# Performance work log

Measured on AMD Instinct MI355X. Metric: run time of the kernel, lower is better.

The kernel has to match this reference:

```python
import jax, jax.numpy as jnp
import numpy as np

B, L, H, N = 4, 4096, 1024, 16
EPS = 1e-6  # layer_norm_epsilon


def setup_inputs() -> dict:
    key = jax.random.key(0)
    ks = jax.random.split(key, 8)
    hidden_states = jax.random.normal(ks[0], (B, L, H), dtype=jnp.float32)
    attention_mask = jnp.ones((B, L), dtype=jnp.float32)
    norm_weight = jnp.ones((H,), dtype=jnp.float32)
    # S4D init: dt log-uniform in [1e-3, 1e-1]; S4D-Lin A init; random C, D
    dt_min, dt_max = 1e-3, 1e-1
    log_dt = jax.random.uniform(ks[1], (H,), dtype=jnp.float32) * (
        float(np.log(dt_max)) - float(np.log(dt_min))) + float(np.log(dt_min))
    log_A_real = jnp.log(0.5 * jnp.ones((H, N), dtype=jnp.float32))
    A_imag = jnp.broadcast_to(float(np.pi) * jnp.arange(N, dtype=jnp.float32), (H, N))
    C_real = jax.random.normal(ks[2], (H, N), dtype=jnp.float32) * (0.5 ** 0.5)
    C_imag = jax.random.normal(ks[3], (H, N), dtype=jnp.float32) * (0.5 ** 0.5)
    D = jax.random.normal(ks[4], (H,), dtype=jnp.float32)
    out_w = jax.random.normal(ks[5], (2 * H, H), dtype=jnp.float32) * 0.02  # 1x1 conv to 2H (GLU)
    out_b = jnp.zeros((2 * H,), dtype=jnp.float32)
    return dict(hidden_states=hidden_states, attention_mask=attention_mask,
                norm_weight=norm_weight, log_dt=log_dt, log_A_real=log_A_real,
                A_imag=A_imag, C_real=C_real, C_imag=C_imag, D=D,
                out_w=out_w, out_b=out_b)


def _s4d_kernel(log_dt, log_A_real, A_imag, C_real, C_imag, length):
    """Diagonal SSM convolution kernel k[h, l] (S4D ZOH discretization)."""
    dt = jnp.exp(log_dt)                                   # (H,)
    A = -jnp.exp(log_A_real) + 1j * A_imag                 # (H, N) complex64
    C = C_real + 1j * C_imag                               # (H, N)
    dtA = A * dt[:, None]                                  # (H, N)
    C_disc = C * (jnp.exp(dtA) - 1.0) / A                  # (H, N)
    vand = jnp.exp(dtA[:, :, None] * jnp.arange(length, dtype=jnp.float32))  # (H, N, L)
    k = 2.0 * jnp.einsum('hn,hnl->hl', C_disc, vand).real  # (H, L)
    return k.astype(jnp.float32)


def reference(hidden_states, attention_mask, norm_weight, log_dt, log_A_real,
              A_imag, C_real, C_imag, D, out_w, out_b):
    # LongT5LayerNorm: RMSNorm (no mean subtraction), variance in fp32
    var = jnp.mean(jnp.square(hidden_states.astype(jnp.float32)), axis=-1, keepdims=True)
    normed = hidden_states * jax.lax.rsqrt(var + EPS) * norm_weight  # (B, L, H)
    # mask padded positions, go to channel-major layout (B, H, L)
    u = (normed * attention_mask[..., None]).transpose(0, 2, 1)
    Lx = u.shape[-1]
    k = _s4d_kernel(log_dt, log_A_real, A_imag, C_real, C_imag, Lx)  # (H, L)
    # causal convolution via FFT of length 2L
    nfft = 2 * Lx
    k_f = jnp.fft.rfft(k, n=nfft)                 # (H, nfft//2+1)
    u_f = jnp.fft.rfft(u, n=nfft)                 # (B, H, nfft//2+1)
    y = jnp.fft.irfft(u_f * k_f, n=nfft)[..., :Lx]  # (B, H, L)
    y = y + u * D[:, None]                        # skip connection
    y = jax.nn.gelu(y, approximate=False)         # torch nn.GELU (exact)
    # output 1x1 conv to 2H, then GLU over the channel dim
    z = jnp.einsum('bhl,oh->bol', y, out_w) + out_b[:, None]
    a, b = jnp.split(z, 2, axis=1)
    ssm_out = (a * jax.nn.sigmoid(b)).transpose(0, 2, 1)  # (B, L, H)
    # residual + dropout (eval mode -> identity)
    return hidden_states + ssm_out
```

## Files before the change

kernel.cpp:

```cpp
#include <hip/hip_runtime.h>

#define B_   4
#define L_   4096
#define H_   1024
#define N_   16
#define CH_  128
#define NC_  (L_/CH_)
#define M_   (B_*L_)
#define O2_  (2*H_)
#define EPS_ 1e-6f

typedef __attribute__((ext_vector_type(4))) float  f32x4;
typedef __attribute__((ext_vector_type(8))) __bf16 bf16x8;

__device__ __forceinline__ unsigned short f2bf(float x) {
  union { float f; unsigned int u; } v; v.f = x;
  unsigned int r = v.u + 0x7FFFu + ((v.u >> 16) & 1u);
  return (unsigned short)(r >> 16);
}

__device__ __forceinline__ void async_copy16(const void* g, void* l) {
  __builtin_amdgcn_global_load_lds(
      (const __attribute__((address_space(1))) unsigned int*)g,
      (__attribute__((address_space(3))) unsigned int*)l, 16, 0, 0);
}

__global__ void k_prep(const float* __restrict__ log_dt,
                       const float* __restrict__ log_A_real,
                       const float* __restrict__ A_imag,
                       const float* __restrict__ C_real,
                       const float* __restrict__ C_imag,
                       const float* __restrict__ outw,
                       const float* __restrict__ outb,
                       float* __restrict__ wr,  float* __restrict__ wi,
                       float* __restrict__ c2r, float* __restrict__ c2i,
                       float* __restrict__ wpr, float* __restrict__ wpi,
                       unsigned short* __restrict__ Wbf,
                       float* __restrict__ bp) {
  int idx = blockIdx.x * 256 + threadIdx.x;
  int p = idx >> 10, hh = idx & (H_ - 1);
  size_t src = (size_t)((p >> 1) + (p & 1) * H_) * H_ + hh;
  Wbf[idx] = f2bf(outw[src]);
  if (idx < O2_) bp[idx] = outb[(idx >> 1) + (idx & 1) * H_];
  if (idx < H_ * N_) {
    int h = idx / N_, n = idx % N_;
    int hn = h * N_ + n;
    float dt  = expf(log_dt[h]);
    float Ar  = -expf(log_A_real[hn]);
    float Ai  = A_imag[hn];
    float dr  = Ar * dt, di = Ai * dt;
    float er  = expf(dr);
    float wrv = er * cosf(di), wiv = er * sinf(di);
    float e1r = wrv - 1.0f, e1i = wiv;
    float den = Ar * Ar + Ai * Ai;
    float qr  = (e1r * Ar + e1i * Ai) / den;
    float qi  = (e1i * Ar - e1r * Ai) / den;
    float Cr  = C_real[hn], Ci = C_imag[hn];
    float cdr = Cr * qr - Ci * qi;
    float cdi = Cr * qi + Ci * qr;
    float ep  = expf((float)CH_ * dr);
    int o = n * H_ + h;
    wr[o]  = wrv;  wi[o]  = wiv;
    c2r[o] = 2.0f * cdr; c2i[o] = 2.0f * cdi;
    wpr[o] = ep * cosf((float)CH_ * di);
    wpi[o] = ep * sinf((float)CH_ * di);
  }
}

__global__ __launch_bounds__(256) void k_scale(const float* __restrict__ hs,
                                               const float* __restrict__ mask,
                                               float* __restrict__ scale) {
  int m = blockIdx.x, tid = threadIdx.x;
  float4 v = reinterpret_cast<const float4*>(hs + (size_t)m * H_)[tid];
  float s = v.x * v.x + v.y * v.y + v.z * v.z + v.w * v.w;
  #pragma unroll
  for (int off = 32; off > 0; off >>= 1) s += __shfl_down(s, off, 64);
  __shared__ float ps[4];
  if ((tid & 63) == 0) ps[tid >> 6] = s;
  __syncthreads();
  if (tid == 0) {
    float var = (ps[0] + ps[1] + ps[2] + ps[3]) * (1.0f / H_);
    scale[m] = rsqrtf(var + EPS_) * mask[m];
  }
}

__global__ __launch_bounds__(256) void k_scan1(const float* __restrict__ hs,
                                               const float* __restrict__ nw,
                                               const float* __restrict__ scale,
                                               const float* __restrict__ wr_,
                                               const float* __restrict__ wi_,
                                               float* __restrict__ endr,
                                               float* __restrict__ endi) {
  int tid = threadIdx.x;
  int h = blockIdx.x * 256 + tid;
  int c = blockIdx.y, b = blockIdx.z;
  float wr[N_], wi[N_], xr[N_], xi[N_];
  #pragma unroll
  for (int n = 0; n < N_; n++) {
    wr[n] = wr_[n * H_ + h]; wi[n] = wi_[n * H_ + h];
    xr[n] = 0.f; xi[n] = 0.f;
  }
  float nwh = nw[h];
  __shared__ float ssc[CH_];
  int l0 = c * CH_;
  if (tid < CH_) ssc[tid] = scale[(size_t)b * L_ + l0 + tid];
  __syncthreads();
  const float* hp = hs + ((size_t)b * L_ + l0) * H_ + h;
  #pragma unroll 8
  for (int l = 0; l < CH_; l++) {
    float u = hp[(size_t)l * H_] * ssc[l] * nwh;
    #pragma unroll
    for (int n = 0; n < N_; n++) {
      float oxr = xr[n];
      xr[n] = fmaf(wr[n], oxr, fmaf(-wi[n], xi[n], u));
      xi[n] = fmaf(wr[n], xi[n], wi[n] * oxr);
    }
  }
  size_t base = (((size_t)b * NC_ + c) * N_) * H_ + h;
  #pragma unroll
  for (int n = 0; n < N_; n++) {
    endr[base + (size_t)n * H_] = xr[n];
    endi[base + (size_t)n * H_] = xi[n];
  }
}

__global__ __launch_bounds__(256) void k_carry(const float* __restrict__ wpr_,
                                               const float* __restrict__ wpi_,
                                               const float* __restrict__ endr,
                                               const float* __restrict__ endi,
                                               float* __restrict__ carr,
                                               float* __restrict__ cari) {
  int idx = blockIdx.x * 256 + threadIdx.x;
  int h = idx & (H_ - 1);
  int n = (idx >> 10) & (N_ - 1);
  int b = idx >> 14;
  float wprv = wpr_[n * H_ + h], wpiv = wpi_[n * H_ + h];
  float sr = 0.f, si = 0.f;
  size_t cstride = (size_t)N_ * H_;
  size_t base = ((size_t)b * NC_) * cstride + (size_t)n * H_ + h;
  for (int c = 0; c < NC_; c++, base += cstride) {
    carr[base] = sr; cari[base] = si;
    float er = endr[base], ei = endi[base];
    float osr = sr;
    sr = fmaf(wprv, osr,  fmaf(-wpiv, si, er));
    si = fmaf(wprv, si, fmaf(wpiv, osr, ei));
  }
}

__global__ __launch_bounds__(256) void k_scan2(const float* __restrict__ hs,
                                               const float* __restrict__ nw,
                                               const float* __restrict__ scale,
                                               const float* __restrict__ wr_,
                                               const float* __restrict__ wi_,
                                               const float* __restrict__ c2r_,
                                               const float* __restrict__ c2i_,
                                               const float* __restrict__ Dp,
                                               const float* __restrict__ carr,
                                               const float* __restrict__ cari,
                                               unsigned short* __restrict__ ybf) {
  int tid = threadIdx.x;
  int h = blockIdx.x * 256 + tid;
  int c = blockIdx.y, b = blockIdx.z;
  float wr[N_], wi[N_], cr[N_], ci[N_], xr[N_], xi[N_];
  size_t base = (((size_t)b * NC_ + c) * N_) * H_ + h;
  #pragma unroll
  for (int n = 0; n < N_; n++) {
    wr[n] = wr_[n * H_ + h]; wi[n] = wi_[n * H_ + h];
    cr[n] = c2r_[n * H_ + h]; ci[n] = c2i_[n * H_ + h];
    xr[n] = carr[base + (size_t)n * H_];
    xi[n] = cari[base + (size_t)n * H_];
  }
  float nwh = nw[h], Dh = Dp[h];
  __shared__ float ssc[CH_];
  int l0 = c * CH_;
  if (tid < CH_) ssc[tid] = scale[(size_t)b * L_ + l0 + tid];
  __syncthreads();
  const float* hp = hs + ((size_t)b * L_ + l0) * H_ + h;
  unsigned short* yp = ybf + ((size_t)b * L_ + l0) * H_ + h;
  #pragma unroll 4
  for (int l = 0; l < CH_; l++) {
    float u = hp[(size_t)l * H_] * ssc[l] * nwh;
    float yv = u * Dh;
    #pragma unroll
    for (int n = 0; n < N_; n++) {
      float oxr = xr[n];
      xr[n] = fmaf(wr[n], oxr, fmaf(-wi[n], xi[n], u));
      xi[n] = fmaf(wr[n], xi[n], wi[n] * oxr);
      yv = fmaf(cr[n], xr[n], yv);
      yv = fmaf(-ci[n], xi[n], yv);
    }
    float g = 0.5f * yv * (1.0f + erff(yv * 0.70710678118654752f));
    yp[(size_t)l * H_] = f2bf(g);
  }
}

#define BM 128
#define BN 128
#define BK 32
__global__ __launch_bounds__(256) void k_gemm(const unsigned short* __restrict__ A,
                                              const unsigned short* __restrict__ Bw,
                                              const float* __restrict__ bp,
                                              const float* __restrict__ hs,
                                              float* __restrict__ out) {
  __shared__ __align__(16) unsigned short As[BM * BK];
  __shared__ __align__(16) unsigned short Bs[BN * BK];
  const int tid  = threadIdx.x;
  const int lane = tid & 63;
  const int wave = tid >> 6;
  const int bn = blockIdx.x * BN;
  const int bm = blockIdx.y * BM;
  const int wm = (wave >> 1) * 64;
  const int wn = (wave & 1) * 64;
  const int K = H_;
  f32x4 acc[4][4];
  #pragma unroll
  for (int mi = 0; mi < 4; mi++)
    #pragma unroll
    for (int ni = 0; ni < 4; ni++) acc[mi][ni] = (f32x4){0.f, 0.f, 0.f, 0.f};

  const int g0 = tid, g1 = 256 + tid;
  const int r0 = g0 >> 2, c0 = ((g0 & 3) ^ ((r0 >> 1) & 3)) * 8;
  const int r1 = g1 >> 2, c1 = ((g1 & 3) ^ ((r1 >> 1) & 3)) * 8;
  const int ar = lane & 15, kqi = lane >> 4;

  for (int k0 = 0; k0 < K; k0 += BK) {
    async_copy16(A  + (size_t)(bm + r0) * K + k0 + c0, &As[g0 * 8]);
    async_copy16(A  + (size_t)(bm + r1) * K + k0 + c1, &As[g1 * 8]);
    async_copy16(Bw + (size_t)(bn + r0) * K + k0 + c0, &Bs[g0 * 8]);
    async_copy16(Bw + (size_t)(bn + r1) * K + k0 + c1, &Bs[g1 * 8]);
    __syncthreads();
    bf16x8 af[4], bf[4];
    #pragma unroll
    for (int mi = 0; mi < 4; mi++) {
      int row = wm + mi * 16 + ar;
      af[mi] = *reinterpret_cast<const bf16x8*>(&As[row * BK + ((kqi ^ ((row >> 1) & 3)) * 8)]);
    }
    #pragma unroll
    for (int ni = 0; ni < 4; ni++) {
      int row = wn + ni * 16 + ar;
      bf[ni] = *reinterpret_cast<const bf16x8*>(&Bs[row * BK + ((kqi ^ ((row >> 1) & 3)) * 8)]);
    }
    #pragma unroll
    for (int mi = 0; mi < 4; mi++)
      #pragma unroll
      for (int ni = 0; ni < 4; ni++)
        acc[mi][ni] = __builtin_amdgcn_mfma_f32_16x16x32_bf16(af[mi], bf[ni], acc[mi][ni], 0, 0, 0);
    __syncthreads();
  }
  #pragma unroll
  for (int mi = 0; mi < 4; mi++) {
    int mrow0 = bm + wm + mi * 16 + (lane >> 4) * 4;
    #pragma unroll
    for (int ni = 0; ni < 4; ni++) {
      int p  = bn + wn + ni * 16 + (lane & 15);
      int pe = p & ~1;
      float bA = bp[pe], bB = bp[pe + 1];
      int j = pe >> 1;
      #pragma unroll
      for (int r = 0; r < 4; r++) {
        float v = acc[mi][ni][r];
        float w = __shfl_xor(v, 1, 64);
        if (!(lane & 1)) {
          float g = (v + bA) / (1.0f + __expf(-(w + bB)));
          size_t o = (size_t)(mrow0 + r) * H_ + j;
          out[o] = hs[o] + g;
        }
      }
    }
  }
}

extern "C" void kernel_launch(void* const* d_in, const int* in_sizes, int n_in,
                              void* d_out, int out_size, void* d_ws, size_t ws_size,
                              hipStream_t stream) {
  const float* hs    = (const float*)d_in[0];
  const float* mask  = (const float*)d_in[1];
  const float* nw    = (const float*)d_in[2];
  const float* ldt   = (const float*)d_in[3];
  const float* lar   = (const float*)d_in[4];
  const float* aim   = (const float*)d_in[5];
  const float* crl   = (const float*)d_in[6];
  const float* cim   = (const float*)d_in[7];
  const float* Dp    = (const float*)d_in[8];
  const float* outw  = (const float*)d_in[9];
  const float* outb  = (const float*)d_in[10];
  float* out = (float*)d_out;

  size_t off = 0;
  char* ws = (char*)d_ws;
  auto nxt = [&](size_t bytes) -> void* {
    void* p = ws + off; off += (bytes + 255) & ~(size_t)255; return p;
  };
  float* wr   = (float*)nxt(H_ * N_ * 4);
  float* wi   = (float*)nxt(H_ * N_ * 4);
  float* c2r  = (float*)nxt(H_ * N_ * 4);
  float* c2i  = (float*)nxt(H_ * N_ * 4);
  float* wpr  = (float*)nxt(H_ * N_ * 4);
  float* wpi  = (float*)nxt(H_ * N_ * 4);
  float* bpck = (float*)nxt(O2_ * 4);
  float* scale= (float*)nxt((size_t)M_ * 4);
  float* endr = (float*)nxt((size_t)B_ * NC_ * N_ * H_ * 4);
  float* endi = (float*)nxt((size_t)B_ * NC_ * N_ * H_ * 4);
  float* carr = (float*)nxt((size_t)B_ * NC_ * N_ * H_ * 4);
  float* cari = (float*)nxt((size_t)B_ * NC_ * N_ * H_ * 4);
  unsigned short* Wbf = (unsigned short*)nxt((size_t)O2_ * H_ * 2);
  unsigned short* ybf = (unsigned short*)nxt((size_t)M_ * H_ * 2);

  k_prep<<<dim3(O2_ * H_ / 256), dim3(256), 0, stream>>>(ldt, lar, aim, crl, cim,
                                                         outw, outb,
                                                         wr, wi, c2r, c2i, wpr, wpi,
                                                         Wbf, bpck);
  k_scale<<<dim3(M_), dim3(256), 0, stream>>>(hs, mask, scale);
  k_scan1<<<dim3(H_ / 256, NC_, B_), dim3(256), 0, stream>>>(hs, nw, scale, wr, wi, endr, endi);
  k_carry<<<dim3(B_ * N_ * H_ / 256), dim3(256), 0, stream>>>(wpr, wpi, endr, endi, carr, cari);
  k_scan2<<<dim3(H_ / 256, NC_, B_), dim3(256), 0, stream>>>(hs, nw, scale, wr, wi, c2r, c2i,
                                                             Dp, carr, cari, ybf);
  k_gemm<<<dim3(O2_ / BN, M_ / BM), dim3(256), 0, stream>>>(ybf, Wbf, bpck, hs, out);
}
```

Measured before the change: 386.5 us.

## Cache bf16 normalized input for second scan, halve chunk size, stage GEMM epilogue

The first scan now writes the normalized, masked input as bf16 to a workspace buffer, and the second scan reads it back instead of re-reading fp32 hidden states and recomputing the scale. This halves the bytes the second scan streams, but both scans now round their input to bf16, which slightly changes accuracy. The chunk length drops from 128 to 64, giving more blocks for parallelism at the cost of a longer carry pass. The GEMM epilogue writes gated results into shared memory first, then does coalesced float4 residual loads and stores instead of strided scalar writes.

```diff
diff --git a/kernel.cpp b/kernel.cpp
--- a/kernel.cpp
+++ b/kernel.cpp
@@ -4,7 +4,7 @@
 #define L_   4096
 #define H_   1024
 #define N_   16
-#define CH_  128
+#define CH_  64
 #define NC_  (L_/CH_)
 #define M_   (B_*L_)
 #define O2_  (2*H_)
@@ -17,6 +17,10 @@
   union { float f; unsigned int u; } v; v.f = x;
   unsigned int r = v.u + 0x7FFFu + ((v.u >> 16) & 1u);
   return (unsigned short)(r >> 16);
+}
+__device__ __forceinline__ float bf2f(unsigned short x) {
+  union { unsigned int u; float f; } v; v.u = ((unsigned int)x) << 16;
+  return v.f;
 }
 
 __device__ __forceinline__ void async_copy16(const void* g, void* l) {
@@ -90,7 +94,8 @@
                                                const float* __restrict__ wr_,
                                                const float* __restrict__ wi_,
                                                float* __restrict__ endr,
-                                               float* __restrict__ endi) {
+                                               float* __restrict__ endi,
+                                               unsigned short* __restrict__ ubf) {
   int tid = threadIdx.x;
   int h = blockIdx.x * 256 + tid;
   int c = blockIdx.y, b = blockIdx.z;
@@ -106,9 +111,13 @@
   if (tid < CH_) ssc[tid] = scale[(size_t)b * L_ + l0 + tid];
   __syncthreads();
   const float* hp = hs + ((size_t)b * L_ + l0) * H_ + h;
+  unsigned short* up = ubf + ((size_t)b * L_ + l0) * H_ + h;
   #pragma unroll 8
   for (int l = 0; l < CH_; l++) {
     float u = hp[(size_t)l * H_] * ssc[l] * nwh;
+    unsigned short ub = f2bf(u);
+    up[(size_t)l * H_] = ub;
+    u = bf2f(ub);
     #pragma unroll
     for (int n = 0; n < N_; n++) {
       float oxr = xr[n];
@@ -147,9 +156,7 @@
   }
 }
 
-__global__ __launch_bounds__(256) void k_scan2(const float* __restrict__ hs,
-                                               const float* __restrict__ nw,
-                                               const float* __restrict__ scale,
+__global__ __launch_bounds__(256) void k_scan2(const unsigned short* __restrict__ ubf,
                                                const float* __restrict__ wr_,
                                                const float* __restrict__ wi_,
                                                const float* __restrict__ c2r_,
@@ -170,16 +177,13 @@
     xr[n] = carr[base + (size_t)n * H_];
     xi[n] = cari[base + (size_t)n * H_];
   }
-  float nwh = nw[h], Dh = Dp[h];
-  __shared__ float ssc[CH_];
+  float Dh = Dp[h];
   int l0 = c * CH_;
-  if (tid < CH_) ssc[tid] = scale[(size_t)b * L_ + l0 + tid];
-  __syncthreads();
-  const float* hp = hs + ((size_t)b * L_ + l0) * H_ + h;
+  const unsigned short* up = ubf + ((size_t)b * L_ + l0) * H_ + h;
   unsigned short* yp = ybf + ((size_t)b * L_ + l0) * H_ + h;
-  #pragma unroll 4
+  #pragma unroll 8
   for (int l = 0; l < CH_; l++) {
-    float u = hp[(size_t)l * H_] * ssc[l] * nwh;
+    float u = bf2f(up[(size_t)l * H_]);
     float yv = u * Dh;
     #pragma unroll
     for (int n = 0; n < N_; n++) {
@@ -197,13 +201,16 @@
 #define BM 128
 #define BN 128
 #define BK 32
+#define GSTRIDE 68
 __global__ __launch_bounds__(256) void k_gemm(const unsigned short* __restrict__ A,
                                               const unsigned short* __restrict__ Bw,
                                               const float* __restrict__ bp,
                                               const float* __restrict__ hs,
                                               float* __restrict__ out) {
-  __shared__ __align__(16) unsigned short As[BM * BK];
-  __shared__ __align__(16) unsigned short Bs[BN * BK];
+  __shared__ __align__(16) char smem[BM * GSTRIDE * 4];
+  unsigned short* As = (unsigned short*)smem;
+  unsigned short* Bs = As + BM * BK;
+  float* gt = (float*)smem;
   const int tid  = threadIdx.x;
   const int lane = tid & 63;
   const int wave = tid >> 6;
@@ -248,24 +255,36 @@
     __syncthreads();
   }
   #pragma unroll
-  for (int mi = 0; mi < 4; mi++) {
-    int mrow0 = bm + wm + mi * 16 + (lane >> 4) * 4;
-    #pragma unroll
-    for (int ni = 0; ni < 4; ni++) {
-      int p  = bn + wn + ni * 16 + (lane & 15);
-      int pe = p & ~1;
-      float bA = bp[pe], bB = bp[pe + 1];
-      int j = pe >> 1;
+  for (int ni = 0; ni < 4; ni++) {
+    int p  = wn + ni * 16 + (lane & 15);
+    int pe = (bn + p) & ~1;
+    float bA = bp[pe], bB = bp[pe + 1];
+    int jl = p >> 1;
+    #pragma unroll
+    for (int mi = 0; mi < 4; mi++) {
+      int row0 = wm + mi * 16 + (lane >> 4) * 4;
       #pragma unroll
       for (int r = 0; r < 4; r++) {
         float v = acc[mi][ni][r];
         float w = __shfl_xor(v, 1, 64);
-        if (!(lane & 1)) {
-          float g = (v + bA) / (1.0f + __expf(-(w + bB)));
-          size_t o = (size_t)(mrow0 + r) * H_ + j;
-          out[o] = hs[o] + g;
-        }
+        if (!(lane & 1))
+          gt[(row0 + r) * GSTRIDE + jl] = (v + bA) / (1.0f + __expf(-(w + bB)));
       }
+    }
+  }
+  __syncthreads();
+  {
+    int c4 = tid & 15;
+    int rr = tid >> 4;
+    size_t obase = (size_t)bm * H_ + (bn >> 1);
+    #pragma unroll
+    for (int rep = 0; rep < 8; rep++) {
+      int row = rep * 16 + rr;
+      float4 g = *reinterpret_cast<const float4*>(&gt[row * GSTRIDE + c4 * 4]);
+      size_t o = obase + (size_t)row * H_ + c4 * 4;
+      float4 hv = *reinterpret_cast<const float4*>(&hs[o]);
+      float4 rv = {hv.x + g.x, hv.y + g.y, hv.z + g.z, hv.w + g.w};
+      *reinterpret_cast<float4*>(&out[o]) = rv;
     }
   }
 }
@@ -304,6 +323,7 @@
   float* carr = (float*)nxt((size_t)B_ * NC_ * N_ * H_ * 4);
   float* cari = (float*)nxt((size_t)B_ * NC_ * N_ * H_ * 4);
   unsigned short* Wbf = (unsigned short*)nxt((size_t)O2_ * H_ * 2);
+  unsigned short* ubf = (unsigned short*)nxt((size_t)M_ * H_ * 2);
   unsigned short* ybf = (unsigned short*)nxt((size_t)M_ * H_ * 2);
 
   k_prep<<<dim3(O2_ * H_ / 256), dim3(256), 0, stream>>>(ldt, lar, aim, crl, cim,
@@ -311,9 +331,10 @@
                                                          wr, wi, c2r, c2i, wpr, wpi,
                                                          Wbf, bpck);
   k_scale<<<dim3(M_), dim3(256), 0, stream>>>(hs, mask, scale);
-  k_scan1<<<dim3(H_ / 256, NC_, B_), dim3(256), 0, stream>>>(hs, nw, scale, wr, wi, endr, endi);
+  k_scan1<<<dim3(H_ / 256, NC_, B_), dim3(256), 0, stream>>>(hs, nw, scale, wr, wi,
+                                                             endr, endi, ubf);
   k_carry<<<dim3(B_ * N_ * H_ / 256), dim3(256), 0, stream>>>(wpr, wpi, endr, endi, carr, cari);
-  k_scan2<<<dim3(H_ / 256, NC_, B_), dim3(256), 0, stream>>>(hs, nw, scale, wr, wi, c2r, c2i,
+  k_scan2<<<dim3(H_ / 256, NC_, B_), dim3(256), 0, stream>>>(ubf, wr, wi, c2r, c2i,
                                                              Dp, carr, cari, ybf);
   k_gemm<<<dim3(O2_ / BN, M_ / BM), dim3(256), 0, stream>>>(ybf, Wbf, bpck, hs, out);
 }
```

New measurement: 366.9 us. -5.1%, faster.
